# Kernel tuning notes

Measured on AMD Instinct MI355X. Metric: run time of the kernel, lower is better.

Reference implementation:

```python
import jax, jax.numpy as jnp
import numpy as np

BRANCH = 4
DEPTH = 5
D = 512
N_NODES = (BRANCH ** (DEPTH + 1) - 1) // (BRANCH - 1)  # 1365
BATCH = 16


def setup_inputs() -> dict:
    key = jax.random.key(0)
    k1, k2, k3 = jax.random.split(key, 3)
    inputs = jax.random.normal(k1, (BATCH, D), dtype=jnp.float32)
    # per-node Linear(512,512) weights, torch layout [out, in], scaled like kaiming-ish init
    W = jax.random.normal(k2, (N_NODES, D, D), dtype=jnp.float32) * (1.0 / np.sqrt(D))
    b = jax.random.normal(k3, (N_NODES, D), dtype=jnp.float32) * 0.01
    return {"inputs": inputs, "W": W, "b": b}


def reference(inputs, W, b):
    # BFS over a complete BRANCH-ary tree; node i>0 has parent (i-1)//BRANCH.
    # Root: Linear only (no relu, per source); children: relu(Linear(parent_act)).
    # All nodes at one BFS level are batched into a single grouped einsum.
    acts = []
    a = inputs @ W[0].T + b[0]          # [B, D] root, no relu
    acts.append(a[:, None, :])
    prev = acts[0]                       # [B, level_size, D]
    prev_start = 0
    start = 1
    for lvl in range(1, DEPTH + 1):
        sz = BRANCH ** lvl
        idx = np.arange(start, start + sz)
        parent_local = (idx - 1) // BRANCH - prev_start  # indices into prev level
        pa = prev[:, parent_local, :]                    # [B, sz, D]
        Wl = W[start:start + sz]                         # [sz, D(out), D(in)]
        bl = b[start:start + sz]                         # [sz, D]
        a = jax.nn.relu(jnp.einsum('bnd,nhd->bnh', pa, Wl) + bl)  # [B, sz, D]
        acts.append(a)
        prev = a
        prev_start = start
        start += sz
    out = jnp.concatenate(acts, axis=1)                  # [B, N_NODES, D]
    return out.reshape(out.shape[0], -1)                 # [B, N_NODES*D], like torch.cat(dim=1)
```

## Files before the change

### kernel.cpp

```cpp
#include <hip/hip_runtime.h>

#define D 512
#define NNODES 1365
#define OUT_STRIDE (NNODES * D)

typedef __attribute__((ext_vector_type(4))) float f32x4;
typedef __attribute__((ext_vector_type(8))) short bf16x8;

union U4 { unsigned u[4]; bf16x8 v; };

__device__ __forceinline__ unsigned cvt_pk_bf16(float s0, float s1) {
    unsigned r;
    asm volatile("v_cvt_pk_bf16_f32 %0, %1, %2" : "=v"(r) : "v"(s0), "v"(s1));
    return r;
}

__device__ __forceinline__ void gld_lds16(const void* g, void* l) {
    __builtin_amdgcn_global_load_lds(
        (const __attribute__((address_space(1))) unsigned*)g,
        (__attribute__((address_space(3))) unsigned*)l, 16, 0, 0);
}

template<int N> __device__ __forceinline__ void waitV() {
    asm volatile("s_waitcnt vmcnt(%0)" :: "i"(N) : "memory");
}

__device__ __forceinline__ void mfma3(bf16x8 ah, bf16x8 al, f32x4 b0, f32x4 b1,
                                      f32x4& acc) {
    U4 bH, bL;
    float xs[8] = {b0[0],b0[1],b0[2],b0[3],b1[0],b1[1],b1[2],b1[3]};
    #pragma unroll
    for (int k = 0; k < 4; ++k) {
        unsigned hh = cvt_pk_bf16(xs[2*k], xs[2*k+1]);
        float f0 = __uint_as_float(hh << 16);
        float f1 = __uint_as_float(hh & 0xFFFF0000u);
        bL.u[k] = cvt_pk_bf16(xs[2*k] - f0, xs[2*k+1] - f1);
        bH.u[k] = hh;
    }
    acc = __builtin_amdgcn_mfma_f32_16x16x32_bf16(ah, bH.v, acc, 0,0,0);
    acc = __builtin_amdgcn_mfma_f32_16x16x32_bf16(al, bH.v, acc, 0,0,0);
    acc = __builtin_amdgcn_mfma_f32_16x16x32_bf16(ah, bL.v, acc, 0,0,0);
}

__device__ __forceinline__ void build_afrags(const float* arow, int m4,
                                             bf16x8* aH, bf16x8* aL) {
    #pragma unroll
    for (int j = 0; j < 16; ++j) {
        const float* p = arow + j * 32 + m4 * 8;
        f32x4 x0 = *(const f32x4*)p;
        f32x4 x1 = *(const f32x4*)(p + 4);
        float xs[8] = {x0[0],x0[1],x0[2],x0[3],x1[0],x1[1],x1[2],x1[3]};
        U4 h, l;
        #pragma unroll
        for (int k = 0; k < 4; ++k) {
            unsigned hh = cvt_pk_bf16(xs[2*k], xs[2*k+1]);
            float f0 = __uint_as_float(hh << 16);
            float f1 = __uint_as_float(hh & 0xFFFF0000u);
            l.u[k] = cvt_pk_bf16(xs[2*k] - f0, xs[2*k+1] - f1);
            h.u[k] = hh;
        }
        aH[j] = h.v; aL[j] = l.v;
    }
}

template<int NGW>
__global__ __launch_bounds__(128)
void stream_kernel(const float* __restrict__ W, const float* __restrict__ bias,
                   const float* __restrict__ src, float* __restrict__ out,
                   int node_start, int bpn)
{
    __shared__ float Wt[2][2][4096];
    __shared__ float bias_lds[32 * NGW];

    const int tid  = threadIdx.x;
    const int w    = tid >> 6;
    const int lane = tid & 63;
    const int m4   = lane >> 4;
    const int c0   = lane & 15;

    const int node  = node_start + blockIdx.x / bpn;
    const int nbase = (blockIdx.x % bpn) * (32 * NGW);
    const char* Wn  = (const char*)(W + (size_t)node * (D * D));

    for (int t = tid; t < 32 * NGW; t += 128)
        bias_lds[t] = bias[(size_t)node * D + nbase + t];

    const float* arow = src + (size_t)c0 * OUT_STRIDE
                            + (size_t)((node - 1) >> 2) * D;
    bf16x8 aH[16], aL[16];
    build_afrags(arow, m4, aH, aL);
    __syncthreads();

    const int u16 = lane * 16;
    auto issue = [&](const char* gchunk, int buf) {
        char* ldst = (char*)&Wt[w][buf][0];
        #pragma unroll
        for (int i = 0; i < 16; ++i)
            gld_lds16(gchunk + (size_t)i * 2048 + (u16 ^ ((i & 7) << 4)),
                      ldst + i * 1024);
    };

    const int rsw = (c0 & 7) << 4;
    const char* tb0 = (const char*)&Wt[w][0][0] + c0 * 1024;
    const char* tb1 = (const char*)&Wt[w][1][0] + c0 * 1024;

    auto half0 = [&](f32x4& acc) {
        #pragma unroll
        for (int ks = 0; ks < 8; ++ks) {
            f32x4 b0 = *(const f32x4*)(tb0 + ((ks * 128 + m4 * 32)      ^ rsw));
            f32x4 b1 = *(const f32x4*)(tb0 + ((ks * 128 + m4 * 32 + 16) ^ rsw));
            mfma3(aH[ks], aL[ks], b0, b1, acc);
        }
    };
    auto half1 = [&](f32x4& acc) {
        #pragma unroll
        for (int ks = 0; ks < 8; ++ks) {
            f32x4 b0 = *(const f32x4*)(tb1 + ((ks * 128 + m4 * 32)      ^ rsw));
            f32x4 b1 = *(const f32x4*)(tb1 + ((ks * 128 + m4 * 32 + 16) ^ rsw));
            mfma3(aH[8 + ks], aL[8 + ks], b0, b1, acc);
        }
    };

    const size_t GSTRIDE = 65536;
    const char* gb = Wn + (size_t)(nbase + w * 16) * 2048;
    issue(gb,        0);
    issue(gb + 1024, 1);

    float* op = out + (size_t)node * D + nbase + w * 16 + c0;
    const float* bl = &bias_lds[w * 16 + c0];

    auto epi = [&](f32x4& acc) {
        const float bv = *bl;
        #pragma unroll
        for (int i = 0; i < 4; ++i)
            op[(size_t)(m4 * 4 + i) * OUT_STRIDE] = fmaxf(acc[i] + bv, 0.f);
        op += 32; bl += 32;
    };

    {
        f32x4 acc = {0.f,0.f,0.f,0.f};
        waitV<16>(); half0(acc);
        issue(gb + GSTRIDE, 0);
        waitV<16>(); half1(acc);
        epi(acc);
        issue(gb + GSTRIDE + 1024, 1);
        gb += GSTRIDE;
    }
    #pragma clang loop unroll(disable)
    for (int g = 1; g < NGW - 1; ++g) {
        f32x4 acc = {0.f,0.f,0.f,0.f};
        waitV<20>(); half0(acc);
        issue(gb + GSTRIDE, 0);
        waitV<16>(); half1(acc);
        epi(acc);
        issue(gb + GSTRIDE + 1024, 1);
        gb += GSTRIDE;
    }
    {
        f32x4 acc = {0.f,0.f,0.f,0.f};
        waitV<20>(); half0(acc);
        waitV<0>();  half1(acc);
        epi(acc);
    }
}

template<bool RELU>
__global__ __launch_bounds__(256, 2)
void node_kernel(const float* __restrict__ W, const float* __restrict__ bias,
                 const float* __restrict__ src_base, float* __restrict__ out,
                 int node_start, int bpn, int ngroups, int src_stride)
{
    __shared__ float Wt[4][2][2048];
    __shared__ float bias_lds[512];

    const int tid  = threadIdx.x;
    const int w    = tid >> 6;
    const int lane = tid & 63;
    const int m4   = lane >> 4;
    const int c0   = lane & 15;

    const int node  = node_start + blockIdx.x / bpn;
    const int nbase = (blockIdx.x % bpn) * (64 * ngroups);
    const char* Wn  = (const char*)(W + (size_t)node * (D * D));

    for (int t = tid; t < 64 * ngroups; t += 256)
        bias_lds[t] = bias[(size_t)node * D + nbase + t];

    const float* arow = (RELU ? src_base + (size_t)((node - 1) >> 2) * D
                              : src_base) + (size_t)c0 * src_stride;
    bf16x8 aH[16], aL[16];
    build_afrags(arow, m4, aH, aL);
    __syncthreads();

    int loffs[8];
    const int rr  = lane >> 5;
    const int off = (lane & 31) * 16;
    #pragma unroll
    for (int i = 0; i < 8; ++i) {
        const int r = i * 2 + rr;
        loffs[i] = r * 2048 + (off ^ ((r & 7) << 4));
    }
    auto issue = [&](const char* gsrc, int buf) {
        char* ldst = (char*)&Wt[w][buf][0];
        #pragma unroll
        for (int i = 0; i < 8; ++i)
            gld_lds16(gsrc + loffs[i], ldst + i * 1024);
    };

    const int rsw = (c0 & 7) << 4;
    const int po0 = c0 * 512 + ((m4 * 32)      ^ rsw);
    const int po1 = c0 * 512 + ((m4 * 32 + 16) ^ rsw);

    const size_t GRP = (size_t)64 * 2048;
    const char* gcur = Wn + (size_t)(nbase + w * 16) * 2048;
    issue(gcur,       0);
    issue(gcur + 512, 1);

    float* optr = out + (size_t)node * D + nbase + w * 16 + c0;
    const float* blds = &bias_lds[w * 16 + c0];

    auto compute_q = [&](auto qc, f32x4& acc) {
        constexpr int Q = decltype(qc)::value;
        const char* tb = (const char*)&Wt[w][Q & 1][0];
        #pragma unroll
        for (int ks = 0; ks < 4; ++ks) {
            f32x4 b0 = *(const f32x4*)(tb + po0 + ks * 128);
            f32x4 b1 = *(const f32x4*)(tb + po1 + ks * 128);
            mfma3(aH[Q*4+ks], aL[Q*4+ks], b0, b1, acc);
        }
    };

    #pragma clang loop unroll(disable)
    for (int g = 0; g < ngroups; ++g) {
        const bool last = (g == ngroups - 1);
        const char* gnext = gcur + GRP;
        f32x4 acc = {0.f,0.f,0.f,0.f};

        waitV<8>();
        compute_q(std::integral_constant<int,0>{}, acc);
        issue(gcur + 1024, 0);
        waitV<8>();
        compute_q(std::integral_constant<int,1>{}, acc);
        issue(gcur + 1536, 1);
        waitV<8>();
        compute_q(std::integral_constant<int,2>{}, acc);
        if (!last) issue(gnext, 0);
        if (last) waitV<0>(); else waitV<8>();
        compute_q(std::integral_constant<int,3>{}, acc);

        const float bv = *blds;
        #pragma unroll
        for (int i = 0; i < 4; ++i) {
            float v = acc[i] + bv;
            if (RELU) v = fmaxf(v, 0.f);
            optr[(size_t)(m4 * 4 + i) * OUT_STRIDE] = v;
        }
        if (!last) issue(gnext + 512, 1);

        gcur = gnext; optr += 64; blds += 64;
    }
}

extern "C" void kernel_launch(void* const* d_in, const int* in_sizes, int n_in,
                              void* d_out, int out_size, void* d_ws, size_t ws_size,
                              hipStream_t stream) {
    const float* inputs = (const float*)d_in[0];
    const float* W      = (const float*)d_in[1];
    const float* bias   = (const float*)d_in[2];
    float* out          = (float*)d_out;

    node_kernel<false><<<   8, 256, 0, stream>>>(W, bias, inputs, out,   0, 8, 1, D);
    node_kernel<true ><<<  32, 256, 0, stream>>>(W, bias, out,    out,   1, 8, 1, OUT_STRIDE);
    node_kernel<true ><<< 128, 256, 0, stream>>>(W, bias, out,    out,   5, 8, 1, OUT_STRIDE);
    node_kernel<true ><<< 512, 256, 0, stream>>>(W, bias, out,    out,  21, 8, 1, OUT_STRIDE);
    stream_kernel< 8><<< 512, 128, 0, stream>>>(W, bias, out, out,  85, 2);
    stream_kernel<16><<<1024, 128, 0, stream>>>(W, bias, out, out, 341, 1);
}
```

Measured before the change: 346.4 us.

## Replace LDS-staged weight streaming with direct per-lane register loads for last levels

The two deepest tree levels now load weight fragments straight from global memory into registers for the MFMA B operands, instead of staging them through swizzled LDS with async global-to-LDS double buffering. Blocks grow to 256 threads, with each wave owning a contiguous slice of output rows, and bias is read directly from global memory. This removes LDS traffic, the LDS bandwidth cost and the explicit waitcnt pipeline. In exchange it relies on the compiler and hardware to hide memory latency, and each lane now issues strided 16-byte loads, which may coalesce less well.

```diff
diff --git a/kernel.cpp b/kernel.cpp
--- a/kernel.cpp
+++ b/kernel.cpp
@@ -64,14 +64,11 @@
 }
 
 template<int NGW>
-__global__ __launch_bounds__(128)
-void stream_kernel(const float* __restrict__ W, const float* __restrict__ bias,
-                   const float* __restrict__ src, float* __restrict__ out,
-                   int node_start, int bpn)
+__global__ __launch_bounds__(256)
+void reg_kernel(const float* __restrict__ W, const float* __restrict__ bias,
+                const float* __restrict__ src, float* __restrict__ out,
+                int node_start, int bpn)
 {
-    __shared__ float Wt[2][2][4096];
-    __shared__ float bias_lds[32 * NGW];
-
     const int tid  = threadIdx.x;
     const int w    = tid >> 6;
     const int lane = tid & 63;
@@ -79,88 +76,39 @@
     const int c0   = lane & 15;
 
     const int node  = node_start + blockIdx.x / bpn;
-    const int nbase = (blockIdx.x % bpn) * (32 * NGW);
+    const int nbase = (blockIdx.x % bpn) * (64 * NGW) + w * (16 * NGW);
     const char* Wn  = (const char*)(W + (size_t)node * (D * D));
-
-    for (int t = tid; t < 32 * NGW; t += 128)
-        bias_lds[t] = bias[(size_t)node * D + nbase + t];
 
     const float* arow = src + (size_t)c0 * OUT_STRIDE
                             + (size_t)((node - 1) >> 2) * D;
     bf16x8 aH[16], aL[16];
     build_afrags(arow, m4, aH, aL);
-    __syncthreads();
-
-    const int u16 = lane * 16;
-    auto issue = [&](const char* gchunk, int buf) {
-        char* ldst = (char*)&Wt[w][buf][0];
-        #pragma unroll
-        for (int i = 0; i < 16; ++i)
-            gld_lds16(gchunk + (size_t)i * 2048 + (u16 ^ ((i & 7) << 4)),
-                      ldst + i * 1024);
-    };
-
-    const int rsw = (c0 & 7) << 4;
-    const char* tb0 = (const char*)&Wt[w][0][0] + c0 * 1024;
-    const char* tb1 = (const char*)&Wt[w][1][0] + c0 * 1024;
-
-    auto half0 = [&](f32x4& acc) {
-        #pragma unroll
-        for (int ks = 0; ks < 8; ++ks) {
-            f32x4 b0 = *(const f32x4*)(tb0 + ((ks * 128 + m4 * 32)      ^ rsw));
-            f32x4 b1 = *(const f32x4*)(tb0 + ((ks * 128 + m4 * 32 + 16) ^ rsw));
-            mfma3(aH[ks], aL[ks], b0, b1, acc);
-        }
-    };
-    auto half1 = [&](f32x4& acc) {
-        #pragma unroll
-        for (int ks = 0; ks < 8; ++ks) {
-            f32x4 b0 = *(const f32x4*)(tb1 + ((ks * 128 + m4 * 32)      ^ rsw));
-            f32x4 b1 = *(const f32x4*)(tb1 + ((ks * 128 + m4 * 32 + 16) ^ rsw));
-            mfma3(aH[8 + ks], aL[8 + ks], b0, b1, acc);
-        }
-    };
-
-    const size_t GSTRIDE = 65536;
-    const char* gb = Wn + (size_t)(nbase + w * 16) * 2048;
-    issue(gb,        0);
-    issue(gb + 1024, 1);
-
-    float* op = out + (size_t)node * D + nbase + w * 16 + c0;
-    const float* bl = &bias_lds[w * 16 + c0];
-
-    auto epi = [&](f32x4& acc) {
-        const float bv = *bl;
+
+    const char*  lanebase = Wn + (size_t)(nbase + c0) * 2048 + m4 * 32;
+    const float* bptr     = bias + (size_t)node * D + nbase + c0;
+    float*       optr     = out  + (size_t)node * D + nbase + c0;
+
+    #pragma clang loop unroll(disable)
+    for (int g = 0; g < NGW; ++g) {
+        const char* gb = lanebase + (size_t)g * 32768;
+        const float bv = bptr[g * 16];
+        f32x4 acc = {0.f, 0.f, 0.f, 0.f};
+        #pragma unroll
+        for (int q = 0; q < 4; ++q) {
+            f32x4 r0[4], r1[4];
+            #pragma unroll
+            for (int k = 0; k < 4; ++k) {
+                r0[k] = *(const f32x4*)(gb + q * 512 + k * 128);
+                r1[k] = *(const f32x4*)(gb + q * 512 + k * 128 + 16);
+            }
+            #pragma unroll
+            for (int k = 0; k < 4; ++k)
+                mfma3(aH[q * 4 + k], aL[q * 4 + k], r0[k], r1[k], acc);
+        }
         #pragma unroll
         for (int i = 0; i < 4; ++i)
-            op[(size_t)(m4 * 4 + i) * OUT_STRIDE] = fmaxf(acc[i] + bv, 0.f);
-        op += 32; bl += 32;
-    };
-
-    {
-        f32x4 acc = {0.f,0.f,0.f,0.f};
-        waitV<16>(); half0(acc);
-        issue(gb + GSTRIDE, 0);
-        waitV<16>(); half1(acc);
-        epi(acc);
-        issue(gb + GSTRIDE + 1024, 1);
-        gb += GSTRIDE;
-    }
-    #pragma clang loop unroll(disable)
-    for (int g = 1; g < NGW - 1; ++g) {
-        f32x4 acc = {0.f,0.f,0.f,0.f};
-        waitV<20>(); half0(acc);
-        issue(gb + GSTRIDE, 0);
-        waitV<16>(); half1(acc);
-        epi(acc);
-        issue(gb + GSTRIDE + 1024, 1);
-        gb += GSTRIDE;
-    }
-    {
-        f32x4 acc = {0.f,0.f,0.f,0.f};
-        waitV<20>(); half0(acc);
-        waitV<0>();  half1(acc);
-        epi(acc);
+            optr[(size_t)(m4 * 4 + i) * OUT_STRIDE + g * 16] =
+                fmaxf(acc[i] + bv, 0.f);
     }
 }
 
@@ -273,6 +221,6 @@
     node_kernel<true ><<<  32, 256, 0, stream>>>(W, bias, out,    out,   1, 8, 1, OUT_STRIDE);
     node_kernel<true ><<< 128, 256, 0, stream>>>(W, bias, out,    out,   5, 8, 1, OUT_STRIDE);
     node_kernel<true ><<< 512, 256, 0, stream>>>(W, bias, out,    out,  21, 8, 1, OUT_STRIDE);
-    stream_kernel< 8><<< 512, 128, 0, stream>>>(W, bias, out, out,  85, 2);
-    stream_kernel<16><<<1024, 128, 0, stream>>>(W, bias, out, out, 341, 1);
-}
+    reg_kernel<4><<< 512, 256, 0, stream>>>(W, bias, out, out,  85, 2);
+    reg_kernel<8><<<1024, 256, 0, stream>>>(W, bias, out, out, 341, 1);
+}
```

After: 362.1 us. +4.5%, slower.
